# Kernel tuning notes

Hardware: AMD Instinct MI355X
Metric: run time of the kernel (lower is better)

## Reference

```python
import jax, jax.numpy as jnp
import numpy as np

B, S, H, NSPAN = 16, 1024, 768, 5
NEG_INF = -1e9


def setup_inputs() -> dict:
    key = jax.random.key(0)
    k1, k2, k3, k4, k5, k6 = jax.random.split(key, 6)
    hidden = jax.random.normal(k1, (B, S, H), dtype=jnp.float32)
    full_emb = jax.random.normal(k2, (B, H), dtype=jnp.float32)
    # nn.Linear weights [out,in] per span head, plus biases and queries
    attn_W = jax.random.normal(k3, (NSPAN, H, H), dtype=jnp.float32) / np.sqrt(H)
    attn_b = jax.random.normal(k4, (NSPAN, H), dtype=jnp.float32) * 0.02
    attn_q = jax.random.uniform(k5, (NSPAN, H), dtype=jnp.float32)  # torch.rand init
    spans = jnp.sort(jax.random.randint(k6, (B, NSPAN, 2), 0, S), axis=-1)
    return {"hidden": hidden, "full_emb": full_emb, "attn_W": attn_W,
            "attn_b": attn_b, "attn_q": attn_q, "spans": spans}


def reference(hidden, full_emb, attn_W, attn_b, attn_q, spans):
    b, s, h = hidden.shape
    starts = spans[..., 0]            # [B,J]
    ends = spans[..., 1]              # [B,J]
    pos = jnp.arange(s)
    mask = (pos[None, None, :] >= starts[..., None]) & (pos[None, None, :] < ends[..., None])  # [B,J,S]
    count = mask.sum(-1)              # [B,J]
    fmask = mask.astype(hidden.dtype)

    # mean pool over each span (zeros when start==end)
    mean = jnp.einsum('bjs,bsh->bjh', fmask, hidden) / jnp.maximum(count, 1).astype(hidden.dtype)[..., None]

    # learned attention pool: tanh(Linear_j(words)), scores vs query_j, softmax over span
    proj = jnp.tanh(jnp.einsum('bsh,joh->bjso', hidden, attn_W) + attn_b[None, :, None, :])  # [B,J,S,H]
    scores = jnp.einsum('jo,bjso->bjs', attn_q, proj)
    scores = jnp.where(mask, scores, NEG_INF)  # max-subtraction in original is a detached shift => identical
    alphas = jax.nn.softmax(scores, axis=-1)
    att = jnp.einsum('bjs,bsh->bjh', alphas, hidden)

    nonempty = (count > 0)[..., None]
    mean = jnp.where(nonempty, mean, 0.0)
    att = jnp.where(nonempty, att, 0.0)

    span_reps = jnp.concatenate([mean, att], axis=-1)          # [B,J,2H], order [mean_j, att_j]
    final = jnp.concatenate([span_reps.reshape(b, -1), full_emb], axis=-1)  # [B, J*2H + H]
    return (final, full_emb)
```

## Files before the change

kernel.cpp:

```cpp
#include <hip/hip_runtime.h>

#define BB 16
#define SS 1024
#define HH 768
#define JJ 5
#define WHJ (HH*HH)
#define RIDX_J (BB*SS)
#define NSEG 4

typedef __attribute__((ext_vector_type(4))) _Float16 h4_t;
typedef __attribute__((ext_vector_type(8))) _Float16 h8_t;
typedef __attribute__((ext_vector_type(4))) float f32x4;

#define WH_HALVES (JJ*HH*HH)
#define WH_BYTES  (WH_HALVES*2)
#define HID_HALVES (BB*SS*HH)
#define HID_BYTES (HID_HALVES*2)
#define SC_FLOATS (BB*JJ*SS)
#define SC_BYTES  (SC_FLOATS*4)
#define RIDX_BYTES (JJ*RIDX_J*4)
#define FINAL_W   (JJ*2*HH + HH)
#define OUT2_OFF  (BB*FINAL_W)

#define NB_CONV (HID_HALVES/4/256)
#define NB_IDX  (JJ*BB)
#define NB_TAIL (BB)

__global__ void k_convert(const float* __restrict__ W, const float* __restrict__ hidden,
                          const float* __restrict__ full_emb, const int* __restrict__ spans,
                          _Float16* __restrict__ Wh, _Float16* __restrict__ Hh,
                          float* __restrict__ scores, int* __restrict__ ridx,
                          int* __restrict__ meta, float* __restrict__ out)
{
    const int bid = blockIdx.x, tid = threadIdx.x;
    __shared__ int cnts[BB];

    if (bid < NB_CONV) {
        int i = bid * 256 + tid;
        {
            float4 v = *(const float4*)(hidden + (size_t)i * 4);
            h4_t hv = { (_Float16)v.x, (_Float16)v.y, (_Float16)v.z, (_Float16)v.w };
            *(h4_t*)(Hh + (size_t)i * 4) = hv;
        }
        if (i < WH_HALVES / 4) {
            float4 v = *(const float4*)(W + (size_t)i * 4);
            h4_t hv = { (_Float16)v.x, (_Float16)v.y, (_Float16)v.z, (_Float16)v.w };
            *(h4_t*)(Wh + (size_t)i * 4) = hv;
        }
        if (i < SC_FLOATS) scores[i] = 0.f;

        if (bid == 0 && tid < 64) {
            int l = tid, l15 = l & 15, lg = l >> 4;
            h8_t a1, b1, a2, b2;
#pragma unroll
            for (int jj = 0; jj < 8; ++jj) {
                int k1 = (jj & 3) + 4 * lg + 16 * (jj >> 2);
                int k2 = jj + 8 * lg;
                a1[jj] = (_Float16)(float)((l15 * 31 + k1 * 17) % 13 - 6);
                b1[jj] = (_Float16)(float)((k1 * 7 + l15 * 5) % 11 - 5);
                a2[jj] = (_Float16)(float)((l15 * 31 + k2 * 17) % 13 - 6);
                b2[jj] = (_Float16)(float)((k2 * 7 + l15 * 5) % 11 - 5);
            }
            f32x4 z = { 0.f, 0.f, 0.f, 0.f };
            f32x4 c1 = __builtin_amdgcn_mfma_f32_16x16x32_f16(a1, b1, z, 0, 0, 0);
            f32x4 c2 = __builtin_amdgcn_mfma_f32_16x16x32_f16(a2, b2, z, 0, 0, 0);
            int ok1 = 1, ok2 = 1;
#pragma unroll
            for (int r = 0; r < 4; ++r) {
                int row = lg * 4 + r;
                float ref = 0.f;
                for (int k = 0; k < 32; ++k)
                    ref += (float)((row * 31 + k * 17) % 13 - 6) *
                           (float)((k * 7 + l15 * 5) % 11 - 5);
                ok1 &= (c1[r] == ref);
                ok2 &= (c2[r] == ref);
            }
            int all1 = __all(ok1);
            int all2 = __all(ok2);
            if (l == 0) meta[5] = all1 ? 1 : (all2 ? 2 : 0);
        }
        return;
    }

    if (bid < NB_CONV + NB_IDX) {
        const int seg = bid - NB_CONV;
        const int j = seg / BB, b = seg % BB;
        if (tid < BB) {
            int st = spans[(tid * JJ + j) * 2 + 0];
            int en = spans[(tid * JJ + j) * 2 + 1];
            cnts[tid] = (en > st) ? (en - st) : 0;
        }
        __syncthreads();
        if (b == 0 && tid == 0) {
            int tot = 0;
            for (int b2 = 0; b2 < BB; ++b2) tot += cnts[b2];
            meta[j] = tot;
        }
        int off = 0;
        for (int b2 = 0; b2 < b; ++b2) off += cnts[b2];
        const int st = spans[(b * JJ + j) * 2 + 0];
        const int cnt = cnts[b];
        const int base = j * RIDX_J + off;
        for (int i = tid; i < cnt; i += 256)
            ridx[base + i] = b * SS + st + i;
        return;
    }

    {
        const int b = bid - NB_CONV - NB_IDX;
        float* ob = out + (size_t)b * FINAL_W;
        for (int h = tid; h < JJ * 2 * HH; h += 256) ob[h] = 0.f;
        for (int h = tid; h < HH; h += 256) {
            float v = full_emb[b * HH + h];
            ob[JJ * 2 * HH + h] = v;
            out[OUT2_OFF + b * HH + h] = v;
        }
    }
}

__device__ __forceinline__ void epilogue(
    f32x4 (&acc)[4][4], const float* qv, const float* bvec, float* scores,
    const int* s_ridx, float* s_red, int j, int nblk, int valid_rows,
    int tid, int wm, int wn, int lg, int l15)
{
    float qn[4], bn[4];
#pragma unroll
    for (int c = 0; c < 4; ++c) {
        int col = nblk * 128 + wn * 64 + c * 16 + l15;
        qn[c] = qv[col];
        bn[c] = bvec[col];
    }
#pragma unroll
    for (int a = 0; a < 4; ++a) {
#pragma unroll
        for (int rr = 0; rr < 4; ++rr) {
            float ssum = 0.f;
#pragma unroll
            for (int c = 0; c < 4; ++c) {
                float yv = acc[a][c][rr] + bn[c];
                yv = fminf(fmaxf(yv, -15.f), 15.f);
                float e = __expf(2.f * yv);
                ssum += qn[c] * ((e - 1.f) / (e + 1.f));
            }
#pragma unroll
            for (int off = 1; off < 16; off <<= 1)
                ssum += __shfl_xor(ssum, off, 64);
            if (l15 == 0)
                s_red[(wm * 2 + wn) * 64 + a * 16 + lg * 4 + rr] = ssum;
        }
    }
    __syncthreads();
    if (tid < valid_rows) {
        int wm2 = tid >> 6, rl = tid & 63;
        float v = s_red[(wm2 * 2) * 64 + rl] + s_red[(wm2 * 2 + 1) * 64 + rl];
        int gidx = s_ridx[tid];
        atomicAdd(&scores[(gidx >> 10) * (JJ * SS) + j * SS + (gidx & 1023)], v);
    }
}

template<int LAYOUT>
__device__ __forceinline__ void scores_reg(
    const _Float16* __restrict__ Hh, const _Float16* __restrict__ wj,
    const float* __restrict__ qv, const float* __restrict__ bvec,
    float* __restrict__ scores, const int* s_ridx,
    _Float16* Alds, _Float16* Blds, float* s_red,
    int j, int nblk, int valid_rows, int tid)
{
    const int r  = tid >> 1, hh = tid & 1;
    const int mf = r >> 4,  mr = r & 15;
    const _Float16* ap = Hh + (size_t)s_ridx[r] * HH + hh * 32;
    const _Float16* bp = wj + (size_t)(nblk * 128 + r) * HH + hh * 32;

    const int wave = tid >> 6, lane = tid & 63;
    const int l15 = lane & 15, lg = lane >> 4;
    const int wm = wave >> 1, wn = wave & 1;

    f32x4 acc[4][4];
#pragma unroll
    for (int a = 0; a < 4; ++a)
#pragma unroll
        for (int c = 0; c < 4; ++c) acc[a][c] = (f32x4){0.f, 0.f, 0.f, 0.f};

    for (int ks = 0; ks < 12; ++ks) {
        h8_t av[4], bv4[4];
        const _Float16* a0 = ap + ks * 64;
        const _Float16* b0 = bp + ks * 64;
#pragma unroll
        for (int g2 = 0; g2 < 4; ++g2) {
            av[g2]  = *(const h8_t*)(a0 + g2 * 8);
            bv4[g2] = *(const h8_t*)(b0 + g2 * 8);
        }
        __syncthreads();
        if (LAYOUT == 2) {
#pragma unroll
            for (int g2 = 0; g2 < 4; ++g2) {
                int c = ((mf * 2 + hh) * 4 + g2) * 16 + mr;
                *(h8_t*)(Alds + c * 8) = av[g2];
                *(h8_t*)(Blds + c * 8) = bv4[g2];
            }
        } else {
#pragma unroll
            for (int g2 = 0; g2 < 4; ++g2) {
                int k0a = g2 * 8, k0b = g2 * 8 + 4;
                int ga = (k0a & 15) >> 2, ja = (k0a >> 4) << 2;
                int gb = (k0b & 15) >> 2, jb = (k0b >> 4) << 2;
                int cA = ((mf * 2 + hh) * 4 + ga) * 16 + mr;
                int cB = ((mf * 2 + hh) * 4 + gb) * 16 + mr;
                h8_t x = av[g2];
                h4_t alo = { x[0], x[1], x[2], x[3] };
                h4_t ahi = { x[4], x[5], x[6], x[7] };
                *(h4_t*)(Alds + cA * 8 + ja) = alo;
                *(h4_t*)(Alds + cB * 8 + jb) = ahi;
                h8_t y = bv4[g2];
                h4_t blo = { y[0], y[1], y[2], y[3] };
                h4_t bhi = { y[4], y[5], y[6], y[7] };
                *(h4_t*)(Blds + cA * 8 + ja) = blo;
                *(h4_t*)(Blds + cB * 8 + jb) = bhi;
            }
        }
        __syncthreads();
#pragma unroll
        for (int ks2 = 0; ks2 < 2; ++ks2) {
            h8_t af[4], bf[4];
#pragma unroll
            for (int f = 0; f < 4; ++f) {
                int ca = (((wm * 4 + f) * 2 + ks2) * 4 + lg) * 16 + l15;
                af[f] = *(const h8_t*)(Alds + ca * 8);
                int cb = (((wn * 4 + f) * 2 + ks2) * 4 + lg) * 16 + l15;
                bf[f] = *(const h8_t*)(Blds + cb * 8);
            }
#pragma unroll
            for (int a = 0; a < 4; ++a)
#pragma unroll
                for (int c = 0; c < 4; ++c)
                    acc[a][c] = __builtin_amdgcn_mfma_f32_16x16x32_f16(
                        af[a], bf[c], acc[a][c], 0, 0, 0);
        }
    }
    epilogue(acc, qv, bvec, scores, s_ridx, s_red, j, nblk, valid_rows,
             tid, wm, wn, lg, l15);
}

__global__ __launch_bounds__(256, 4) void k_scores(
    const _Float16* __restrict__ Hh, const _Float16* __restrict__ Wh,
    const float* __restrict__ attn_b, const float* __restrict__ attn_q,
    float* __restrict__ scores, const int* __restrict__ ridx,
    const int* __restrict__ meta)
{
    const int tile = blockIdx.x, nblk = blockIdx.y, j = blockIdx.z;
    const int Mj = meta[j];
    const int rows_base = tile * 128;
    if (rows_base >= Mj) return;
    const int valid_rows = min(128, Mj - rows_base);

    __shared__ __align__(16) _Float16 Alds[1024 * 8];
    __shared__ __align__(16) _Float16 Blds[1024 * 8];
    __shared__ int   s_ridx[128];
    __shared__ float s_red[256];

    const int tid = threadIdx.x;
    if (tid < 128)
        s_ridx[tid] = ridx[j * RIDX_J + rows_base + min(tid, valid_rows - 1)];
    __syncthreads();

    const _Float16* wj = Wh + (size_t)j * WHJ;
    const float* qv = attn_q + j * HH;
    const float* bv = attn_b + j * HH;

    if (meta[5] == 2)
        scores_reg<2>(Hh, wj, qv, bv, scores, s_ridx, Alds, Blds, s_red,
                      j, nblk, valid_rows, tid);
    else
        scores_reg<1>(Hh, wj, qv, bv, scores, s_ridx, Alds, Blds, s_red,
                      j, nblk, valid_rows, tid);
}

__global__ __launch_bounds__(256) void k_pool(
    const _Float16* __restrict__ Hh, const float* __restrict__ scores,
    const int* __restrict__ spans, float* __restrict__ out)
{
    const int bj = blockIdx.x, seg = blockIdx.y;
    const int b = bj / JJ, j = bj % JJ;
    const int start = spans[bj * 2 + 0];
    const int end   = spans[bj * 2 + 1];
    const int count = end - start;
    if (count <= 0) return;

    const int tid = threadIdx.x;
    const float* sc = scores + bj * SS;
    __shared__ float red[8];
    __shared__ float wl[257];

    float lm = -3.0e38f;
    for (int s = start + tid; s < end; s += 256) lm = fmaxf(lm, sc[s]);
#pragma unroll
    for (int off = 32; off > 0; off >>= 1) lm = fmaxf(lm, __shfl_xor(lm, off, 64));
    int wid = tid >> 6, lane = tid & 63;
    if (lane == 0) red[wid] = lm;
    __syncthreads();
    float m = fmaxf(fmaxf(red[0], red[1]), fmaxf(red[2], red[3]));

    float ld = 0.f;
    for (int s = start + tid; s < end; s += 256) ld += __expf(sc[s] - m);
#pragma unroll
    for (int off = 32; off > 0; off >>= 1) ld += __shfl_xor(ld, off, 64);
    if (lane == 0) red[4 + wid] = ld;
    __syncthreads();
    float inv_d = 1.f / (red[4] + red[5] + red[6] + red[7]);

    const int i0 = start + (count * seg) / NSEG;
    const int i1 = start + (count * (seg + 1)) / NSEG;
    for (int s = i0 + tid; s < i1; s += 256)
        wl[s - i0] = __expf(sc[s] - m) * inv_d;
    __syncthreads();

    if (tid < 192) {
        float am[4] = {0.f, 0.f, 0.f, 0.f}, aa[4] = {0.f, 0.f, 0.f, 0.f};
        const _Float16* hp = Hh + (size_t)b * SS * HH + tid * 4;
        const int n = i1 - i0;
        int i = 0;
        for (; i + 4 <= n; i += 4) {
            h4_t v0 = *(const h4_t*)(hp + (size_t)(i0 + i + 0) * HH);
            h4_t v1 = *(const h4_t*)(hp + (size_t)(i0 + i + 1) * HH);
            h4_t v2 = *(const h4_t*)(hp + (size_t)(i0 + i + 2) * HH);
            h4_t v3 = *(const h4_t*)(hp + (size_t)(i0 + i + 3) * HH);
            float w0 = wl[i], w1 = wl[i + 1], w2 = wl[i + 2], w3 = wl[i + 3];
#pragma unroll
            for (int c = 0; c < 4; ++c) {
                float x0 = (float)v0[c], x1 = (float)v1[c];
                float x2 = (float)v2[c], x3 = (float)v3[c];
                am[c] += (x0 + x1) + (x2 + x3);
                aa[c] += (w0 * x0 + w1 * x1) + (w2 * x2 + w3 * x3);
            }
        }
        for (; i < n; ++i) {
            h4_t v = *(const h4_t*)(hp + (size_t)(i0 + i) * HH);
            float w = wl[i];
#pragma unroll
            for (int c = 0; c < 4; ++c) {
                float x = (float)v[c];
                am[c] += x;
                aa[c] += w * x;
            }
        }
        float inv = 1.f / (float)count;
        float* fin = out + (size_t)b * FINAL_W + j * (2 * HH);
#pragma unroll
        for (int c = 0; c < 4; ++c) {
            atomicAdd(&fin[tid * 4 + c], am[c] * inv);
            atomicAdd(&fin[HH + tid * 4 + c], aa[c]);
        }
    }
}

extern "C" void kernel_launch(void* const* d_in, const int* in_sizes, int n_in,
                              void* d_out, int out_size, void* d_ws, size_t ws_size,
                              hipStream_t stream)
{
    const float* hidden   = (const float*)d_in[0];
    const float* full_emb = (const float*)d_in[1];
    const float* attn_W   = (const float*)d_in[2];
    const float* attn_b   = (const float*)d_in[3];
    const float* attn_q   = (const float*)d_in[4];
    const int*   spans    = (const int*)d_in[5];
    float* out = (float*)d_out;

    char* ws = (char*)d_ws;
    _Float16* Wh  = (_Float16*)ws;
    _Float16* Hh  = (_Float16*)(ws + WH_BYTES);
    float* scores = (float*)(ws + WH_BYTES + HID_BYTES);
    int*   ridx   = (int*)(ws + WH_BYTES + HID_BYTES + SC_BYTES);
    int*   meta   = (int*)(ws + WH_BYTES + HID_BYTES + SC_BYTES + RIDX_BYTES);

    k_convert<<<NB_CONV + NB_IDX + NB_TAIL, 256, 0, stream>>>(
        attn_W, hidden, full_emb, spans, Wh, Hh, scores, ridx, meta, out);
    k_scores<<<dim3(RIDX_J / 128, HH / 128, JJ), 256, 0, stream>>>(
        Hh, Wh, attn_b, attn_q, scores, ridx, meta);
    k_pool<<<dim3(BB * JJ, NSEG), 256, 0, stream>>>(Hh, scores, spans, out);
}
```

Measured before the change: 119.3 us.

## Load MFMA operands directly from global memory and remap blocks across XCDs

The GEMM in k_scores no longer stages A and B tiles through shared memory with two barriers per k-step. Each lane now gathers its MFMA fragments straight from global memory (L2/L1), which removes the LDS traffic and the synchronisation. The launch also changes from a 3D grid to a 1D grid whose block index is remapped so consecutive work items land on the same XCD, aiming for better L2 reuse of the weight and hidden tiles. The risk is many more narrow global loads that are less coalesced (16-byte loads per row), plus heavier reliance on cache hit rates.

New measurement: 428.3 us. 3.59x slower.

```diff
diff --git a/kernel.cpp b/kernel.cpp
--- a/kernel.cpp
+++ b/kernel.cpp
@@ -26,6 +26,10 @@
 #define NB_IDX  (JJ*BB)
 #define NB_TAIL (BB)
 
+#define NTILE   (RIDX_J/128)
+#define NBLKN   (HH/128)
+#define NWORK   (JJ*NTILE*NBLKN)
+
 __global__ void k_convert(const float* __restrict__ W, const float* __restrict__ hidden,
                           const float* __restrict__ full_emb, const int* __restrict__ spans,
                           _Float16* __restrict__ Wh, _Float16* __restrict__ Hh,
@@ -159,83 +163,61 @@
 }
 
 template<int LAYOUT>
-__device__ __forceinline__ void scores_reg(
+__device__ __forceinline__ void scores_direct(
     const _Float16* __restrict__ Hh, const _Float16* __restrict__ wj,
     const float* __restrict__ qv, const float* __restrict__ bvec,
-    float* __restrict__ scores, const int* s_ridx,
-    _Float16* Alds, _Float16* Blds, float* s_red,
+    float* __restrict__ scores, const int* s_ridx, float* s_red,
     int j, int nblk, int valid_rows, int tid)
 {
-    const int r  = tid >> 1, hh = tid & 1;
-    const int mf = r >> 4,  mr = r & 15;
-    const _Float16* ap = Hh + (size_t)s_ridx[r] * HH + hh * 32;
-    const _Float16* bp = wj + (size_t)(nblk * 128 + r) * HH + hh * 32;
-
     const int wave = tid >> 6, lane = tid & 63;
     const int l15 = lane & 15, lg = lane >> 4;
     const int wm = wave >> 1, wn = wave & 1;
 
+    const _Float16* pA[4];
+    const _Float16* pB[4];
+#pragma unroll
+    for (int f = 0; f < 4; ++f) {
+        pA[f] = Hh + (size_t)s_ridx[wm * 64 + f * 16 + l15] * HH;
+        pB[f] = wj + (size_t)(nblk * 128 + wn * 64 + f * 16 + l15) * HH;
+    }
+
     f32x4 acc[4][4];
 #pragma unroll
     for (int a = 0; a < 4; ++a)
 #pragma unroll
         for (int c = 0; c < 4; ++c) acc[a][c] = (f32x4){0.f, 0.f, 0.f, 0.f};
 
-    for (int ks = 0; ks < 12; ++ks) {
-        h8_t av[4], bv4[4];
-        const _Float16* a0 = ap + ks * 64;
-        const _Float16* b0 = bp + ks * 64;
-#pragma unroll
-        for (int g2 = 0; g2 < 4; ++g2) {
-            av[g2]  = *(const h8_t*)(a0 + g2 * 8);
-            bv4[g2] = *(const h8_t*)(b0 + g2 * 8);
-        }
-        __syncthreads();
+    for (int ks = 0; ks < 24; ++ks) {
+        h8_t af[4], bf[4];
         if (LAYOUT == 2) {
-#pragma unroll
-            for (int g2 = 0; g2 < 4; ++g2) {
-                int c = ((mf * 2 + hh) * 4 + g2) * 16 + mr;
-                *(h8_t*)(Alds + c * 8) = av[g2];
-                *(h8_t*)(Blds + c * 8) = bv4[g2];
+            const int koff = ks * 32 + lg * 8;
+#pragma unroll
+            for (int f = 0; f < 4; ++f) {
+                af[f] = *(const h8_t*)(pA[f] + koff);
+                bf[f] = *(const h8_t*)(pB[f] + koff);
             }
         } else {
-#pragma unroll
-            for (int g2 = 0; g2 < 4; ++g2) {
-                int k0a = g2 * 8, k0b = g2 * 8 + 4;
-                int ga = (k0a & 15) >> 2, ja = (k0a >> 4) << 2;
-                int gb = (k0b & 15) >> 2, jb = (k0b >> 4) << 2;
-                int cA = ((mf * 2 + hh) * 4 + ga) * 16 + mr;
-                int cB = ((mf * 2 + hh) * 4 + gb) * 16 + mr;
-                h8_t x = av[g2];
-                h4_t alo = { x[0], x[1], x[2], x[3] };
-                h4_t ahi = { x[4], x[5], x[6], x[7] };
-                *(h4_t*)(Alds + cA * 8 + ja) = alo;
-                *(h4_t*)(Alds + cB * 8 + jb) = ahi;
-                h8_t y = bv4[g2];
-                h4_t blo = { y[0], y[1], y[2], y[3] };
-                h4_t bhi = { y[4], y[5], y[6], y[7] };
-                *(h4_t*)(Blds + cA * 8 + ja) = blo;
-                *(h4_t*)(Blds + cB * 8 + jb) = bhi;
-            }
-        }
-        __syncthreads();
-#pragma unroll
-        for (int ks2 = 0; ks2 < 2; ++ks2) {
-            h8_t af[4], bf[4];
+            const int klo = ks * 32 + lg * 4, khi = ks * 32 + 16 + lg * 4;
 #pragma unroll
             for (int f = 0; f < 4; ++f) {
-                int ca = (((wm * 4 + f) * 2 + ks2) * 4 + lg) * 16 + l15;
-                af[f] = *(const h8_t*)(Alds + ca * 8);
-                int cb = (((wn * 4 + f) * 2 + ks2) * 4 + lg) * 16 + l15;
-                bf[f] = *(const h8_t*)(Blds + cb * 8);
-            }
-#pragma unroll
-            for (int a = 0; a < 4; ++a)
-#pragma unroll
-                for (int c = 0; c < 4; ++c)
-                    acc[a][c] = __builtin_amdgcn_mfma_f32_16x16x32_f16(
-                        af[a], bf[c], acc[a][c], 0, 0, 0);
-        }
+                h4_t alo = *(const h4_t*)(pA[f] + klo);
+                h4_t ahi = *(const h4_t*)(pA[f] + khi);
+                h4_t blo = *(const h4_t*)(pB[f] + klo);
+                h4_t bhi = *(const h4_t*)(pB[f] + khi);
+                h8_t ta, tb;
+                ta[0]=alo[0]; ta[1]=alo[1]; ta[2]=alo[2]; ta[3]=alo[3];
+                ta[4]=ahi[0]; ta[5]=ahi[1]; ta[6]=ahi[2]; ta[7]=ahi[3];
+                tb[0]=blo[0]; tb[1]=blo[1]; tb[2]=blo[2]; tb[3]=blo[3];
+                tb[4]=bhi[0]; tb[5]=bhi[1]; tb[6]=bhi[2]; tb[7]=bhi[3];
+                af[f] = ta; bf[f] = tb;
+            }
+        }
+#pragma unroll
+        for (int a = 0; a < 4; ++a)
+#pragma unroll
+            for (int c = 0; c < 4; ++c)
+                acc[a][c] = __builtin_amdgcn_mfma_f32_16x16x32_f16(
+                    af[a], bf[c], acc[a][c], 0, 0, 0);
     }
     epilogue(acc, qv, bvec, scores, s_ridx, s_red, j, nblk, valid_rows,
              tid, wm, wn, lg, l15);
@@ -247,14 +229,17 @@
     float* __restrict__ scores, const int* __restrict__ ridx,
     const int* __restrict__ meta)
 {
-    const int tile = blockIdx.x, nblk = blockIdx.y, j = blockIdx.z;
+    const int xcd = blockIdx.x & 7, idx = blockIdx.x >> 3;
+    const int work = xcd * (NWORK / 8) + idx;
+    const int j    = work / (NTILE * NBLKN);
+    const int rem  = work - j * (NTILE * NBLKN);
+    const int tile = rem / NBLKN, nblk = rem % NBLKN;
+
     const int Mj = meta[j];
     const int rows_base = tile * 128;
     if (rows_base >= Mj) return;
     const int valid_rows = min(128, Mj - rows_base);
 
-    __shared__ __align__(16) _Float16 Alds[1024 * 8];
-    __shared__ __align__(16) _Float16 Blds[1024 * 8];
     __shared__ int   s_ridx[128];
     __shared__ float s_red[256];
 
@@ -268,11 +253,11 @@
     const float* bv = attn_b + j * HH;
 
     if (meta[5] == 2)
-        scores_reg<2>(Hh, wj, qv, bv, scores, s_ridx, Alds, Blds, s_red,
-                      j, nblk, valid_rows, tid);
+        scores_direct<2>(Hh, wj, qv, bv, scores, s_ridx, s_red,
+                         j, nblk, valid_rows, tid);
     else
-        scores_reg<1>(Hh, wj, qv, bv, scores, s_ridx, Alds, Blds, s_red,
-                      j, nblk, valid_rows, tid);
+        scores_direct<1>(Hh, wj, qv, bv, scores, s_ridx, s_red,
+                         j, nblk, valid_rows, tid);
 }
 
 __global__ __launch_bounds__(256) void k_pool(
@@ -374,7 +359,7 @@
 
     k_convert<<<NB_CONV + NB_IDX + NB_TAIL, 256, 0, stream>>>(
         attn_W, hidden, full_emb, spans, Wh, Hh, scores, ridx, meta, out);
-    k_scores<<<dim3(RIDX_J / 128, HH / 128, JJ), 256, 0, stream>>>(
+    k_scores<<<NWORK, 256, 0, stream>>>(
         Hh, Wh, attn_b, attn_q, scores, ridx, meta);
     k_pool<<<dim3(BB * JJ, NSEG), 256, 0, stream>>>(Hh, scores, spans, out);
 }
```

## Load weight MFMA fragments directly from global memory, skipping LDS staging

Applied to the files above, without the earlier changes.

The scores GEMM no longer stages the weight tile in shared memory. Each wave now reads its B fragments straight from global memory (or L2) into registers, in MFMA operand order. The hidden-state A tile is still staged in LDS. This halves LDS use, which may raise occupancy, and removes the B LDS writes and reads. The cost is uncoalesced 16-byte global loads that are repeated across the two wm waves and issued right before the MFMAs, so there is little latency hiding.

Measured after the change: 243.8 us. +104.4%, slower.

```diff
diff --git a/kernel.cpp b/kernel.cpp
--- a/kernel.cpp
+++ b/kernel.cpp
@@ -159,22 +159,26 @@
 }
 
 template<int LAYOUT>
-__device__ __forceinline__ void scores_reg(
+__device__ __forceinline__ void scores_hyb(
     const _Float16* __restrict__ Hh, const _Float16* __restrict__ wj,
     const float* __restrict__ qv, const float* __restrict__ bvec,
     float* __restrict__ scores, const int* s_ridx,
-    _Float16* Alds, _Float16* Blds, float* s_red,
+    _Float16* Alds, float* s_red,
     int j, int nblk, int valid_rows, int tid)
 {
     const int r  = tid >> 1, hh = tid & 1;
     const int mf = r >> 4,  mr = r & 15;
     const _Float16* ap = Hh + (size_t)s_ridx[r] * HH + hh * 32;
-    const _Float16* bp = wj + (size_t)(nblk * 128 + r) * HH + hh * 32;
 
     const int wave = tid >> 6, lane = tid & 63;
     const int l15 = lane & 15, lg = lane >> 4;
     const int wm = wave >> 1, wn = wave & 1;
 
+    const _Float16* pB[4];
+#pragma unroll
+    for (int f = 0; f < 4; ++f)
+        pB[f] = wj + (size_t)(nblk * 128 + wn * 64 + f * 16 + l15) * HH;
+
     f32x4 acc[4][4];
 #pragma unroll
     for (int a = 0; a < 4; ++a)
@@ -182,21 +186,17 @@
         for (int c = 0; c < 4; ++c) acc[a][c] = (f32x4){0.f, 0.f, 0.f, 0.f};
 
     for (int ks = 0; ks < 12; ++ks) {
-        h8_t av[4], bv4[4];
+        h8_t av[4];
         const _Float16* a0 = ap + ks * 64;
-        const _Float16* b0 = bp + ks * 64;
-#pragma unroll
-        for (int g2 = 0; g2 < 4; ++g2) {
-            av[g2]  = *(const h8_t*)(a0 + g2 * 8);
-            bv4[g2] = *(const h8_t*)(b0 + g2 * 8);
-        }
+#pragma unroll
+        for (int g2 = 0; g2 < 4; ++g2)
+            av[g2] = *(const h8_t*)(a0 + g2 * 8);
         __syncthreads();
         if (LAYOUT == 2) {
 #pragma unroll
             for (int g2 = 0; g2 < 4; ++g2) {
                 int c = ((mf * 2 + hh) * 4 + g2) * 16 + mr;
                 *(h8_t*)(Alds + c * 8) = av[g2];
-                *(h8_t*)(Blds + c * 8) = bv4[g2];
             }
         } else {
 #pragma unroll
@@ -211,11 +211,6 @@
                 h4_t ahi = { x[4], x[5], x[6], x[7] };
                 *(h4_t*)(Alds + cA * 8 + ja) = alo;
                 *(h4_t*)(Alds + cB * 8 + jb) = ahi;
-                h8_t y = bv4[g2];
-                h4_t blo = { y[0], y[1], y[2], y[3] };
-                h4_t bhi = { y[4], y[5], y[6], y[7] };
-                *(h4_t*)(Blds + cA * 8 + ja) = blo;
-                *(h4_t*)(Blds + cB * 8 + jb) = bhi;
             }
         }
         __syncthreads();
@@ -226,8 +221,24 @@
             for (int f = 0; f < 4; ++f) {
                 int ca = (((wm * 4 + f) * 2 + ks2) * 4 + lg) * 16 + l15;
                 af[f] = *(const h8_t*)(Alds + ca * 8);
-                int cb = (((wn * 4 + f) * 2 + ks2) * 4 + lg) * 16 + l15;
-                bf[f] = *(const h8_t*)(Blds + cb * 8);
+            }
+            if (LAYOUT == 2) {
+                const int koff = ks * 64 + ks2 * 32 + lg * 8;
+#pragma unroll
+                for (int f = 0; f < 4; ++f)
+                    bf[f] = *(const h8_t*)(pB[f] + koff);
+            } else {
+                const int klo = ks * 64 + ks2 * 32 + lg * 4;
+                const int khi = klo + 16;
+#pragma unroll
+                for (int f = 0; f < 4; ++f) {
+                    h4_t blo = *(const h4_t*)(pB[f] + klo);
+                    h4_t bhi = *(const h4_t*)(pB[f] + khi);
+                    h8_t tb;
+                    tb[0]=blo[0]; tb[1]=blo[1]; tb[2]=blo[2]; tb[3]=blo[3];
+                    tb[4]=bhi[0]; tb[5]=bhi[1]; tb[6]=bhi[2]; tb[7]=bhi[3];
+                    bf[f] = tb;
+                }
             }
 #pragma unroll
             for (int a = 0; a < 4; ++a)
@@ -254,7 +265,6 @@
     const int valid_rows = min(128, Mj - rows_base);
 
     __shared__ __align__(16) _Float16 Alds[1024 * 8];
-    __shared__ __align__(16) _Float16 Blds[1024 * 8];
     __shared__ int   s_ridx[128];
     __shared__ float s_red[256];
 
@@ -268,10 +278,10 @@
     const float* bv = attn_b + j * HH;
 
     if (meta[5] == 2)
-        scores_reg<2>(Hh, wj, qv, bv, scores, s_ridx, Alds, Blds, s_red,
+        scores_hyb<2>(Hh, wj, qv, bv, scores, s_ridx, Alds, s_red,
                       j, nblk, valid_rows, tid);
     else
-        scores_reg<1>(Hh, wj, qv, bv, scores, s_ridx, Alds, Blds, s_red,
+        scores_hyb<1>(Hh, wj, qv, bv, scores, s_ridx, Alds, s_red,
                       j, nblk, valid_rows, tid);
 }
 
```

## Double-buffer global loads in score GEMM and double pool segments

Applied to the files above, without the earlier changes.

The score GEMM main loop now keeps two register sets and issues the global loads for the next K-slice before writing and computing the current one. This hides global memory latency behind the MFMA work. It also doubles NSEG from 4 to 8, splitting the pooling kernel across more blocks, and resizes the shared weight buffer to match. The cost is extra register pressure under launch_bounds(256,4), which could cause spills or lower occupancy.

Measured after the change: 315.2 us. +164.3%, slower.

```diff
diff --git a/kernel.cpp b/kernel.cpp
--- a/kernel.cpp
+++ b/kernel.cpp
@@ -6,7 +6,7 @@
 #define JJ 5
 #define WHJ (HH*HH)
 #define RIDX_J (BB*SS)
-#define NSEG 4
+#define NSEG 8
 
 typedef __attribute__((ext_vector_type(4))) _Float16 h4_t;
 typedef __attribute__((ext_vector_type(8))) _Float16 h8_t;
@@ -158,6 +158,69 @@
     }
 }
 
+#define LOADS(KS, AV, BV)                                                \
+    do {                                                                 \
+        const _Float16* a0_ = ap + (KS) * 64;                            \
+        const _Float16* b0_ = bp + (KS) * 64;                            \
+        _Pragma("unroll")                                                \
+        for (int g2_ = 0; g2_ < 4; ++g2_) {                              \
+            AV[g2_] = *(const h8_t*)(a0_ + g2_ * 8);                     \
+            BV[g2_] = *(const h8_t*)(b0_ + g2_ * 8);                     \
+        }                                                                \
+    } while (0)
+
+#define WRITES(AV, BV)                                                   \
+    do {                                                                 \
+        if (LAYOUT == 2) {                                               \
+            _Pragma("unroll")                                            \
+            for (int g2_ = 0; g2_ < 4; ++g2_) {                          \
+                int c_ = ((mf * 2 + hh) * 4 + g2_) * 16 + mr;            \
+                *(h8_t*)(Alds + c_ * 8) = AV[g2_];                       \
+                *(h8_t*)(Blds + c_ * 8) = BV[g2_];                       \
+            }                                                            \
+        } else {                                                         \
+            _Pragma("unroll")                                            \
+            for (int g2_ = 0; g2_ < 4; ++g2_) {                          \
+                int k0a_ = g2_ * 8, k0b_ = g2_ * 8 + 4;                  \
+                int ga_ = (k0a_ & 15) >> 2, ja_ = (k0a_ >> 4) << 2;      \
+                int gb_ = (k0b_ & 15) >> 2, jb_ = (k0b_ >> 4) << 2;      \
+                int cA_ = ((mf * 2 + hh) * 4 + ga_) * 16 + mr;           \
+                int cB_ = ((mf * 2 + hh) * 4 + gb_) * 16 + mr;           \
+                h8_t x_ = AV[g2_];                                       \
+                h4_t alo_ = { x_[0], x_[1], x_[2], x_[3] };              \
+                h4_t ahi_ = { x_[4], x_[5], x_[6], x_[7] };              \
+                *(h4_t*)(Alds + cA_ * 8 + ja_) = alo_;                   \
+                *(h4_t*)(Alds + cB_ * 8 + jb_) = ahi_;                   \
+                h8_t y_ = BV[g2_];                                       \
+                h4_t blo_ = { y_[0], y_[1], y_[2], y_[3] };              \
+                h4_t bhi_ = { y_[4], y_[5], y_[6], y_[7] };              \
+                *(h4_t*)(Blds + cA_ * 8 + ja_) = blo_;                   \
+                *(h4_t*)(Blds + cB_ * 8 + jb_) = bhi_;                   \
+            }                                                            \
+        }                                                                \
+    } while (0)
+
+#define COMPUTE()                                                        \
+    do {                                                                 \
+        _Pragma("unroll")                                                \
+        for (int ks2_ = 0; ks2_ < 2; ++ks2_) {                           \
+            h8_t af_[4], bf_[4];                                         \
+            _Pragma("unroll")                                            \
+            for (int f_ = 0; f_ < 4; ++f_) {                             \
+                int ca_ = (((wm * 4 + f_) * 2 + ks2_) * 4 + lg) * 16 + l15; \
+                af_[f_] = *(const h8_t*)(Alds + ca_ * 8);                \
+                int cb_ = (((wn * 4 + f_) * 2 + ks2_) * 4 + lg) * 16 + l15; \
+                bf_[f_] = *(const h8_t*)(Blds + cb_ * 8);                \
+            }                                                            \
+            _Pragma("unroll")                                            \
+            for (int a_ = 0; a_ < 4; ++a_)                               \
+                _Pragma("unroll")                                        \
+                for (int c_ = 0; c_ < 4; ++c_)                           \
+                    acc[a_][c_] = __builtin_amdgcn_mfma_f32_16x16x32_f16(\
+                        af_[a_], bf_[c_], acc[a_][c_], 0, 0, 0);         \
+        }                                                                \
+    } while (0)
+
 template<int LAYOUT>
 __device__ __forceinline__ void scores_reg(
     const _Float16* __restrict__ Hh, const _Float16* __restrict__ wj,
@@ -181,61 +244,19 @@
 #pragma unroll
         for (int c = 0; c < 4; ++c) acc[a][c] = (f32x4){0.f, 0.f, 0.f, 0.f};
 
-    for (int ks = 0; ks < 12; ++ks) {
-        h8_t av[4], bv4[4];
-        const _Float16* a0 = ap + ks * 64;
-        const _Float16* b0 = bp + ks * 64;
-#pragma unroll
-        for (int g2 = 0; g2 < 4; ++g2) {
-            av[g2]  = *(const h8_t*)(a0 + g2 * 8);
-            bv4[g2] = *(const h8_t*)(b0 + g2 * 8);
-        }
+    h8_t avA[4], bvA[4], avB[4], bvB[4];
+    LOADS(0, avA, bvA);
+    for (int ks = 0; ks < 12; ks += 2) {
+        LOADS(ks + 1, avB, bvB);
         __syncthreads();
-        if (LAYOUT == 2) {
-#pragma unroll
-            for (int g2 = 0; g2 < 4; ++g2) {
-                int c = ((mf * 2 + hh) * 4 + g2) * 16 + mr;
-                *(h8_t*)(Alds + c * 8) = av[g2];
-                *(h8_t*)(Blds + c * 8) = bv4[g2];
-            }
-        } else {
-#pragma unroll
-            for (int g2 = 0; g2 < 4; ++g2) {
-                int k0a = g2 * 8, k0b = g2 * 8 + 4;
-                int ga = (k0a & 15) >> 2, ja = (k0a >> 4) << 2;
-                int gb = (k0b & 15) >> 2, jb = (k0b >> 4) << 2;
-                int cA = ((mf * 2 + hh) * 4 + ga) * 16 + mr;
-                int cB = ((mf * 2 + hh) * 4 + gb) * 16 + mr;
-                h8_t x = av[g2];
-                h4_t alo = { x[0], x[1], x[2], x[3] };
-                h4_t ahi = { x[4], x[5], x[6], x[7] };
-                *(h4_t*)(Alds + cA * 8 + ja) = alo;
-                *(h4_t*)(Alds + cB * 8 + jb) = ahi;
-                h8_t y = bv4[g2];
-                h4_t blo = { y[0], y[1], y[2], y[3] };
-                h4_t bhi = { y[4], y[5], y[6], y[7] };
-                *(h4_t*)(Blds + cA * 8 + ja) = blo;
-                *(h4_t*)(Blds + cB * 8 + jb) = bhi;
-            }
-        }
+        WRITES(avA, bvA);
         __syncthreads();
-#pragma unroll
-        for (int ks2 = 0; ks2 < 2; ++ks2) {
-            h8_t af[4], bf[4];
-#pragma unroll
-            for (int f = 0; f < 4; ++f) {
-                int ca = (((wm * 4 + f) * 2 + ks2) * 4 + lg) * 16 + l15;
-                af[f] = *(const h8_t*)(Alds + ca * 8);
-                int cb = (((wn * 4 + f) * 2 + ks2) * 4 + lg) * 16 + l15;
-                bf[f] = *(const h8_t*)(Blds + cb * 8);
-            }
-#pragma unroll
-            for (int a = 0; a < 4; ++a)
-#pragma unroll
-                for (int c = 0; c < 4; ++c)
-                    acc[a][c] = __builtin_amdgcn_mfma_f32_16x16x32_f16(
-                        af[a], bf[c], acc[a][c], 0, 0, 0);
-        }
+        COMPUTE();
+        if (ks + 2 < 12) LOADS(ks + 2, avA, bvA);
+        __syncthreads();
+        WRITES(avB, bvB);
+        __syncthreads();
+        COMPUTE();
     }
     epilogue(acc, qv, bvec, scores, s_ridx, s_red, j, nblk, valid_rows,
              tid, wm, wn, lg, l15);
@@ -289,7 +310,7 @@
     const int tid = threadIdx.x;
     const float* sc = scores + bj * SS;
     __shared__ float red[8];
-    __shared__ float wl[257];
+    __shared__ float wl[SS / NSEG + 1];
 
     float lm = -3.0e38f;
     for (int s = start + tid; s < end; s += 256) lm = fmaxf(lm, sc[s]);
```
